# Kernel tuning notes

Measured on AMD Instinct MI355X. Metric: run time of the kernel, lower is better.

Reference implementation:

```python
import jax, jax.numpy as jnp
import numpy as np

D = 32       # hidden_size (hardcoded in AR.__init__)
H = 16       # num_heads
HD = D // H  # head_dim = 2
L = 8        # num DiT blocks
MLP = 128    # mlp_ratio 4.0
B, S, T, P = 16, 1024, 256, 32
SCALE = float(1.0 / np.sqrt(HD))


def _ln(x, g, b, eps=1e-6):
    mu = jnp.mean(x, axis=-1, keepdims=True)
    var = jnp.mean((x - mu) ** 2, axis=-1, keepdims=True)
    return (x - mu) * jax.lax.rsqrt(var + eps) * g + b


def _mha(q_in, kv_in, in_w, in_b, out_w, out_b):
    # nn.MultiheadAttention math, batch-first layout (permutation-equivalent)
    wq, wk, wv = in_w[:D], in_w[D:2 * D], in_w[2 * D:]
    bq, bk, bv = in_b[:D], in_b[D:2 * D], in_b[2 * D:]
    Bq, Sq = q_in.shape[0], q_in.shape[1]
    Sk = kv_in.shape[1]
    q = (q_in @ wq.T + bq).reshape(Bq, Sq, H, HD)
    k = (kv_in @ wk.T + bk).reshape(Bq, Sk, H, HD)
    v = (kv_in @ wv.T + bv).reshape(Bq, Sk, H, HD)
    scores = jnp.einsum('bqhd,bkhd->bhqk', q, k) * SCALE
    a = jax.nn.softmax(scores, axis=-1)
    o = jnp.einsum('bhqk,bkhd->bqhd', a, v).reshape(Bq, Sq, D)
    return o @ out_w.T + out_b


def setup_inputs() -> dict:
    key = jax.random.key(0)
    ks = iter(jax.random.split(key, 40))
    rn = lambda k, sh, sc=1.0: jax.random.normal(k, sh, jnp.float32) * sc
    inp = {
        'x': rn(next(ks), (B, S, D)),
        'speaker_emb': rn(next(ks), (B, P, D)),
        'text_phonemes': rn(next(ks), (B, T, D)),
        'timestep_emb': rn(next(ks), (B, D)),
        'mask': jnp.ones((S,), jnp.float32),
        # per-block params, stacked over L for lax.scan
        'ln1_g': jnp.ones((L, D)), 'ln1_b': jnp.zeros((L, D)),
        'ln2_g': jnp.ones((L, D)), 'ln2_b': jnp.zeros((L, D)),
        'ln22_g': jnp.ones((L, D)), 'ln22_b': jnp.zeros((L, D)),
        'ln3_g': jnp.ones((L, D)), 'ln3_b': jnp.zeros((L, D)),
        'attn_in_w': rn(next(ks), (L, 3 * D, D), 0.1), 'attn_in_b': jnp.zeros((L, 3 * D)),
        'attn_out_w': rn(next(ks), (L, D, D), 0.1), 'attn_out_b': jnp.zeros((L, D)),
        'cross_in_w': rn(next(ks), (L, 3 * D, D), 0.1), 'cross_in_b': jnp.zeros((L, 3 * D)),
        'cross_out_w': rn(next(ks), (L, D, D), 0.1), 'cross_out_b': jnp.zeros((L, D)),
        'ts_w': rn(next(ks), (L, 2 * D, D), 0.1), 'ts_b': jnp.zeros((L, 2 * D)),
        'fc1_w': rn(next(ks), (L, MLP, D), 0.1), 'fc1_b': jnp.zeros((L, MLP)),
        'fc2_w': rn(next(ks), (L, D, MLP), 0.1), 'fc2_b': jnp.zeros((L, D)),
    }
    return inp


def _forward(x, speaker_emb, text_phonemes, timestep_emb, mask, params):
    m = mask[None, :, None]  # (1, S, 1), matches mask.unsqueeze(0).unsqueeze(2)
    def body(h, p):
        h = h * m
        hn = _ln(h, p['ln1_g'], p['ln1_b'])
        h = h + _mha(hn, hn, p['attn_in_w'], p['attn_in_b'], p['attn_out_w'], p['attn_out_b'])
        # both cross attentions use cross_attn weights (cross_attn2 is dead code in source)
        ca1 = _mha(_ln(h, p['ln2_g'], p['ln2_b']), text_phonemes,
                   p['cross_in_w'], p['cross_in_b'], p['cross_out_w'], p['cross_out_b'])
        ca2 = _mha(_ln(h, p['ln22_g'], p['ln22_b']), speaker_emb,
                   p['cross_in_w'], p['cross_in_b'], p['cross_out_w'], p['cross_out_b'])
        h = h + ca1 + ca2
        ss = timestep_emb @ p['ts_w'].T + p['ts_b']        # (B, 2D)
        scale, shift = ss[:, :D], ss[:, D:]
        hm = _ln(h, p['ln3_g'], p['ln3_b']) * (1.0 + scale[:, None, :]) + shift[:, None, :]
        mlp = jax.nn.gelu(hm @ p['fc1_w'].T + p['fc1_b'], approximate=False) @ p['fc2_w'].T + p['fc2_b']
        return (h + mlp) * m, None
    out, _ = jax.lax.scan(body, x, params)
    return out


def reference(x, speaker_emb, text_phonemes, timestep_emb, mask,
              ln1_g, ln1_b, ln2_g, ln2_b, ln22_g, ln22_b, ln3_g, ln3_b,
              attn_in_w, attn_in_b, attn_out_w, attn_out_b,
              cross_in_w, cross_in_b, cross_out_w, cross_out_b,
              ts_w, ts_b, fc1_w, fc1_b, fc2_w, fc2_b):
    params = dict(ln1_g=ln1_g, ln1_b=ln1_b, ln2_g=ln2_g, ln2_b=ln2_b,
                  ln22_g=ln22_g, ln22_b=ln22_b, ln3_g=ln3_g, ln3_b=ln3_b,
                  attn_in_w=attn_in_w, attn_in_b=attn_in_b,
                  attn_out_w=attn_out_w, attn_out_b=attn_out_b,
                  cross_in_w=cross_in_w, cross_in_b=cross_in_b,
                  cross_out_w=cross_out_w, cross_out_b=cross_out_b,
                  ts_w=ts_w, ts_b=ts_b, fc1_w=fc1_w, fc1_b=fc1_b,
                  fc2_w=fc2_w, fc2_b=fc2_b)
    return _forward(x, speaker_emb, text_phonemes, timestep_emb, mask, params)
```

## Files before the change

kernel.cpp:

```cpp
#include <hip/hip_runtime.h>
#include <math.h>

#define NB 16
#define SEQ 1024
#define NT 16384
#define TT 256
#define PP 32
#define NL 8
#define SCALE 0.70710678118654752f
#define LOG2E 1.4426950408889634f
#define CS (SCALE * LOG2E)

static __device__ __forceinline__ float exp2fast(float x) {
#if __has_builtin(__builtin_amdgcn_exp2f)
  return __builtin_amdgcn_exp2f(x);
#else
  return exp2f(x);
#endif
}

__global__ __launch_bounds__(256) void k_pre(const float* __restrict__ tse,
                                             const float* __restrict__ tsw,
                                             const float* __restrict__ tsb,
                                             float* __restrict__ ssa,
                                             const float* __restrict__ text,
                                             const float* __restrict__ spk,
                                             const float* __restrict__ cw,
                                             const float* __restrict__ cb,
                                             float* __restrict__ kvtT,
                                             float* __restrict__ kvsT) {
  __shared__ float sh[64 * 33];
  int tid = threadIdx.x;
  int bx = blockIdx.x;
  if (bx < 32) {
    int idx = bx * 256 + tid;
    int l = idx >> 10;
    int rem = idx & 1023;
    int b = rem >> 6;
    int j = rem & 63;
    const float* wr = tsw + ((size_t)l * 64 + j) * 32;
    const float* xr = tse + b * 32;
    float acc = tsb[l * 64 + j];
#pragma unroll
    for (int e = 0; e < 32; e++) acc = fmaf(xr[e], wr[e], acc);
    ssa[idx] = acc;
    return;
  }
  const float* src;
  float* dst;
  int l, tok0, ntok;
  if (bx < 544) {
    l = (bx - 32) >> 6; tok0 = ((bx - 32) & 63) * 64; ntok = NB * TT; src = text;
    dst = kvtT + (size_t)l * 64 * ntok;
  } else {
    l = (bx - 544) >> 3; tok0 = ((bx - 544) & 7) * 64; ntok = NB * PP; src = spk;
    dst = kvsT + (size_t)l * 64 * ntok;
  }
  const float* w = cw + (size_t)l * 96 * 32 + 32 * 32;
  const float* wb = cb + (size_t)l * 96 + 32;
  for (int i = tid; i < 64 * 32; i += 256) {
    int tl = i >> 5, e = i & 31;
    sh[tl * 33 + e] = src[(size_t)(tok0 + tl) * 32 + e];
  }
  __syncthreads();
  int tl = tid & 63;
  int wv = tid >> 6;
#pragma unroll
  for (int k = 0; k < 16; k++) {
    int j = __builtin_amdgcn_readfirstlane(wv + 4 * k);
    const float* wr = w + j * 32;
    const float* hr = sh + tl * 33;
    float acc = wb[j];
#pragma unroll
    for (int e = 0; e < 32; e++) acc = fmaf(hr[e], wr[e], acc);
    dst[(size_t)j * ntok + tok0 + tl] = acc;
  }
}

__device__ __forceinline__ void load_row32(const float* __restrict__ base, int tok, float* r) {
#pragma unroll
  for (int e = 0; e < 32; e++) r[e] = base[(size_t)e * NT + tok];
}

__device__ __forceinline__ void ln_core(float* r) {
  float a0 = 0, a1 = 0, a2 = 0, a3 = 0;
#pragma unroll
  for (int e = 0; e < 32; e += 4) { a0 += r[e]; a1 += r[e + 1]; a2 += r[e + 2]; a3 += r[e + 3]; }
  float mu = ((a0 + a1) + (a2 + a3)) * (1.0f / 32.0f);
  float v0 = 0, v1 = 0, v2 = 0, v3 = 0;
#pragma unroll
  for (int e = 0; e < 32; e += 4) {
    float d0 = r[e] - mu, d1 = r[e + 1] - mu, d2 = r[e + 2] - mu, d3 = r[e + 3] - mu;
    v0 = fmaf(d0, d0, v0); v1 = fmaf(d1, d1, v1); v2 = fmaf(d2, d2, v2); v3 = fmaf(d3, d3, v3);
  }
  float rstd = rsqrtf(((v0 + v1) + (v2 + v3)) * (1.0f / 32.0f) + 1e-6f);
#pragma unroll
  for (int e = 0; e < 32; e++) r[e] = (r[e] - mu) * rstd;
}

__global__ __launch_bounds__(256) void k_qkv(const float* __restrict__ hin,
                                             int rowmajor,
                                             float* __restrict__ hT,
                                             const float* __restrict__ mask,
                                             const float* __restrict__ w,
                                             const float* __restrict__ wb,
                                             const float* __restrict__ g,
                                             const float* __restrict__ bv,
                                             float* __restrict__ qkvT) {
  int tid = threadIdx.x;
  int tok0 = blockIdx.x * 64;
  int yc = blockIdx.y;
  int tl = tid & 63, wv = tid >> 6;
  int tok = tok0 + tl;
  float r[32];
  if (rowmajor) {
    float m = mask[tok & (SEQ - 1)];
#pragma unroll
    for (int e = 0; e < 32; e++) r[e] = hin[(size_t)tok * 32 + e] * m;
    if (yc == 0 && wv == 0) {
#pragma unroll
      for (int e = 0; e < 32; e++) hT[(size_t)e * NT + tok] = r[e];
    }
  } else {
    load_row32(hin, tok, r);
  }
  ln_core(r);
#pragma unroll
  for (int e = 0; e < 32; e++) r[e] = fmaf(r[e], g[e], bv[e]);
#pragma unroll
  for (int k = 0; k < 6; k++) {
    int j = __builtin_amdgcn_readfirstlane(yc * 24 + wv + 4 * k);
    const float* wr = w + j * 32;
    float acc = wb[j];
#pragma unroll
    for (int e = 0; e < 32; e++) acc = fmaf(r[e], wr[e], acc);
    qkvT[(size_t)j * NT + tok] = acc;
  }
}

__global__ __launch_bounds__(256) void k_q12(const float* __restrict__ hT,
                                             const float* __restrict__ w,
                                             const float* __restrict__ wb,
                                             const float* __restrict__ g2, const float* __restrict__ b2,
                                             const float* __restrict__ g22, const float* __restrict__ b22,
                                             float* __restrict__ q1T, float* __restrict__ q2T) {
  int tid = threadIdx.x;
  int tok0 = blockIdx.x * 64, yc = blockIdx.y;
  int tl = tid & 63, wv = tid >> 6;
  int tok = tok0 + tl;
  float r[32];
  load_row32(hT, tok, r);
  ln_core(r);
  const float* g = (yc >= 2) ? g22 : g2;
  const float* bb = (yc >= 2) ? b22 : b2;
  float* dst = (yc >= 2) ? q2T : q1T;
#pragma unroll
  for (int e = 0; e < 32; e++) r[e] = fmaf(r[e], g[e], bb[e]);
  int jbase = (yc & 1) * 16;
#pragma unroll
  for (int k = 0; k < 4; k++) {
    int j = __builtin_amdgcn_readfirstlane(jbase + wv + 4 * k);
    const float* wr = w + j * 32;
    float acc = wb[j];
#pragma unroll
    for (int e = 0; e < 32; e++) acc = fmaf(r[e], wr[e], acc);
    dst[(size_t)j * NT + tok] = acc;
  }
}

__global__ __launch_bounds__(256) void k_proj_add(const float* __restrict__ s1T,
                                                  const float* __restrict__ s2T,
                                                  const float* __restrict__ w,
                                                  const float* __restrict__ wb, float bmult,
                                                  float* __restrict__ hT) {
  int tid = threadIdx.x;
  int tok0 = blockIdx.x * 64, yc = blockIdx.y;
  int tl = tid & 63, wv = tid >> 6;
  int tok = tok0 + tl;
  float r[32];
  if (s2T) {
#pragma unroll
    for (int e = 0; e < 32; e++)
      r[e] = s1T[(size_t)e * NT + tok] + s2T[(size_t)e * NT + tok];
  } else {
    load_row32(s1T, tok, r);
  }
#pragma unroll
  for (int k = 0; k < 2; k++) {
    int j = __builtin_amdgcn_readfirstlane(yc * 8 + wv + 4 * k);
    const float* wr = w + j * 32;
    float acc = bmult * wb[j];
#pragma unroll
    for (int e = 0; e < 32; e++) acc = fmaf(r[e], wr[e], acc);
    size_t gi = (size_t)j * NT + tok;
    hT[gi] += acc;
  }
}

template <int SK, int SETS>
__device__ __forceinline__ void attn_core(const float* __restrict__ qb,
                                          const float* __restrict__ kb,
                                          const float* __restrict__ vb,
                                          int kvld,
                                          float* __restrict__ ob) {
  constexpr int RPW = 4 * SETS;
  constexpr int RPB = 4 * RPW;
  constexpr int NRC = SEQ / RPB;
  int tid = threadIdx.x;
  int bx = blockIdx.x;
  int rc = bx % NRC, bh = bx / NRC;
  int b = bh >> 4, hh = bh & 15;
  int wv = tid >> 6, lane = tid & 63;
  int rg = lane >> 4, kl = lane & 15;
  int rbase = rc * RPB + wv * RPW + rg;

  const float* qxp = qb + (size_t)(2 * hh) * NT + b * SEQ;
  const float* qyp = qxp + NT;
  const float* kx = kb + (size_t)(2 * hh) * kvld + b * SK;
  const float* ky = kx + kvld;
  const float* vx = vb + (size_t)(2 * hh) * kvld + b * SK;
  const float* vy = vx + kvld;

  float qx[SETS], qy[SETS], sum[SETS], ox[SETS], oy[SETS];
#pragma unroll
  for (int s = 0; s < SETS; s++) {
    qx[s] = qxp[rbase + 4 * s] * CS;
    qy[s] = qyp[rbase + 4 * s] * CS;
    sum[s] = 0.f; ox[s] = 0.f; oy[s] = 0.f;
  }

  if constexpr (SK >= 64) {
#pragma unroll 2
    for (int c = 0; c < SK / 64; c++) {
      int o = c * 64 + kl * 4;
      float4 k4x = *(const float4*)(kx + o);
      float4 k4y = *(const float4*)(ky + o);
      float4 v4x = *(const float4*)(vx + o);
      float4 v4y = *(const float4*)(vy + o);
#pragma unroll
      for (int s = 0; s < SETS; s++) {
        float e0 = exp2fast(fmaf(qy[s], k4y.x, qx[s] * k4x.x));
        float e1 = exp2fast(fmaf(qy[s], k4y.y, qx[s] * k4x.y));
        float e2 = exp2fast(fmaf(qy[s], k4y.z, qx[s] * k4x.z));
        float e3 = exp2fast(fmaf(qy[s], k4y.w, qx[s] * k4x.w));
        sum[s] += (e0 + e1) + (e2 + e3);
        ox[s] = fmaf(e0, v4x.x, ox[s]);
        ox[s] = fmaf(e1, v4x.y, ox[s]);
        ox[s] = fmaf(e2, v4x.z, ox[s]);
        ox[s] = fmaf(e3, v4x.w, ox[s]);
        oy[s] = fmaf(e0, v4y.x, oy[s]);
        oy[s] = fmaf(e1, v4y.y, oy[s]);
        oy[s] = fmaf(e2, v4y.z, oy[s]);
        oy[s] = fmaf(e3, v4y.w, oy[s]);
      }
    }
  } else {
    float2 k2x = *(const float2*)(kx + kl * 2);
    float2 k2y = *(const float2*)(ky + kl * 2);
    float2 v2x = *(const float2*)(vx + kl * 2);
    float2 v2y = *(const float2*)(vy + kl * 2);
#pragma unroll
    for (int s = 0; s < SETS; s++) {
      float e0 = exp2fast(fmaf(qy[s], k2y.x, qx[s] * k2x.x));
      float e1 = exp2fast(fmaf(qy[s], k2y.y, qx[s] * k2x.y));
      sum[s] += e0 + e1;
      ox[s] = fmaf(e0, v2x.x, ox[s]);
      ox[s] = fmaf(e1, v2x.y, ox[s]);
      oy[s] = fmaf(e0, v2y.x, oy[s]);
      oy[s] = fmaf(e1, v2y.y, oy[s]);
    }
  }

  float* oxr = ob + (size_t)(2 * hh) * NT + b * SEQ;
  float* oyr = oxr + NT;
#pragma unroll
  for (int s = 0; s < SETS; s++) {
    float sm = sum[s];
    float o1 = ox[s];
    float o2 = oy[s];
#pragma unroll
    for (int off = 1; off < 16; off <<= 1) {
      sm += __shfl_xor(sm, off);
      o1 += __shfl_xor(o1, off);
      o2 += __shfl_xor(o2, off);
    }
    if (kl == 0) {
      float inv = 1.0f / sm;
      int r = rbase + 4 * s;
      oxr[r] = o1 * inv;
      oyr[r] = o2 * inv;
    }
  }
}

__global__ __launch_bounds__(256) void k_attn_self(const float* __restrict__ qkvT,
                                                   float* __restrict__ oT) {
  attn_core<SEQ, 8>(qkvT, qkvT + (size_t)32 * NT, qkvT + (size_t)64 * NT, NT, oT);
}

__global__ __launch_bounds__(256) void k_attn_cross(const float* __restrict__ q1T,
                                                    const float* __restrict__ q2T,
                                                    const float* __restrict__ kvt,
                                                    const float* __restrict__ kvs,
                                                    float* __restrict__ o1T,
                                                    float* __restrict__ o2T) {
  if (blockIdx.y == 0)
    attn_core<TT, 8>(q1T, kvt, kvt + (size_t)32 * (NB * TT), NB * TT, o1T);
  else
    attn_core<PP, 8>(q2T, kvs, kvs + (size_t)32 * (NB * PP), NB * PP, o2T);
}

__global__ __launch_bounds__(256) void k_fc1(const float* __restrict__ hT,
                                             const float* __restrict__ ssl,
                                             const float* __restrict__ g, const float* __restrict__ bv,
                                             const float* __restrict__ w1, const float* __restrict__ b1,
                                             float* __restrict__ uT) {
  int tid = threadIdx.x;
  int tok0 = blockIdx.x * 64, yc = blockIdx.y;
  int tl = tid & 63, wv = tid >> 6;
  int tok = tok0 + tl;
  int b = tok0 >> 10;
  const float* sc = ssl + b * 64;
  float r[32];
  load_row32(hT, tok, r);
  ln_core(r);
#pragma unroll
  for (int e = 0; e < 32; e++) {
    float ln = fmaf(r[e], g[e], bv[e]);
    r[e] = fmaf(ln, 1.0f + sc[e], sc[32 + e]);
  }
#pragma unroll
  for (int k = 0; k < 8; k++) {
    int j = __builtin_amdgcn_readfirstlane(yc * 32 + wv + 4 * k);
    const float* wr = w1 + j * 32;
    float acc = b1[j];
#pragma unroll
    for (int e = 0; e < 32; e++) acc = fmaf(r[e], wr[e], acc);
    float ge = 0.5f * acc * (1.0f + erff(acc * 0.70710678118654752f));
    uT[(size_t)j * NT + tok] = ge;
  }
}

__global__ __launch_bounds__(256) void k_fc2(const float* __restrict__ uT,
                                             float* hT,
                                             float* __restrict__ out_rm,
                                             const float* __restrict__ mask,
                                             const float* __restrict__ w2,
                                             const float* __restrict__ b2) {
  __shared__ __align__(16) float shu[64 * 132];
  int tid = threadIdx.x;
  int tok0 = blockIdx.x * 64, yc = blockIdx.y;
  for (int i = tid; i < 64 * 128; i += 256) {
    int e = i >> 6, tl = i & 63;
    shu[tl * 132 + e] = uT[(size_t)e * NT + tok0 + tl];
  }
  __syncthreads();
  int tl = tid & 63, wv = tid >> 6;
  int tok = tok0 + tl;
  int j0 = __builtin_amdgcn_readfirstlane(yc * 16 + wv);
  int j1 = __builtin_amdgcn_readfirstlane(j0 + 4);
  int j2 = __builtin_amdgcn_readfirstlane(j0 + 8);
  int j3 = __builtin_amdgcn_readfirstlane(j0 + 12);
  const float* w0 = w2 + j0 * 128;
  const float* w1 = w2 + j1 * 128;
  const float* w2r = w2 + j2 * 128;
  const float* w3 = w2 + j3 * 128;
  float a0 = b2[j0], a1 = b2[j1], a2 = b2[j2], a3 = b2[j3];
  const float4* ur = (const float4*)(shu + tl * 132);
#pragma unroll
  for (int m = 0; m < 32; m++) {
    float4 t = ur[m];
    a0 = fmaf(t.x, w0[4 * m], a0); a0 = fmaf(t.y, w0[4 * m + 1], a0);
    a0 = fmaf(t.z, w0[4 * m + 2], a0); a0 = fmaf(t.w, w0[4 * m + 3], a0);
    a1 = fmaf(t.x, w1[4 * m], a1); a1 = fmaf(t.y, w1[4 * m + 1], a1);
    a1 = fmaf(t.z, w1[4 * m + 2], a1); a1 = fmaf(t.w, w1[4 * m + 3], a1);
    a2 = fmaf(t.x, w2r[4 * m], a2); a2 = fmaf(t.y, w2r[4 * m + 1], a2);
    a2 = fmaf(t.z, w2r[4 * m + 2], a2); a2 = fmaf(t.w, w2r[4 * m + 3], a2);
    a3 = fmaf(t.x, w3[4 * m], a3); a3 = fmaf(t.y, w3[4 * m + 1], a3);
    a3 = fmaf(t.z, w3[4 * m + 2], a3); a3 = fmaf(t.w, w3[4 * m + 3], a3);
  }
  float mk = mask[tok & (SEQ - 1)];
  size_t g0 = (size_t)j0 * NT + tok, g1 = (size_t)j1 * NT + tok;
  size_t g2i = (size_t)j2 * NT + tok, g3 = (size_t)j3 * NT + tok;
  float r0 = (hT[g0] + a0) * mk;
  float r1 = (hT[g1] + a1) * mk;
  float r2 = (hT[g2i] + a2) * mk;
  float r3 = (hT[g3] + a3) * mk;
  if (out_rm) {
    out_rm[(size_t)tok * 32 + j0] = r0;
    out_rm[(size_t)tok * 32 + j1] = r1;
    out_rm[(size_t)tok * 32 + j2] = r2;
    out_rm[(size_t)tok * 32 + j3] = r3;
  } else {
    hT[g0] = r0;
    hT[g1] = r1;
    hT[g2i] = r2;
    hT[g3] = r3;
  }
}

extern "C" void kernel_launch(void* const* d_in, const int* in_sizes, int n_in,
                              void* d_out, int out_size, void* d_ws, size_t ws_size,
                              hipStream_t stream) {
  const float* x = (const float*)d_in[0];
  const float* spk = (const float*)d_in[1];
  const float* text = (const float*)d_in[2];
  const float* tse = (const float*)d_in[3];
  const float* mask = (const float*)d_in[4];
  const float* ln1_g = (const float*)d_in[5];
  const float* ln1_b = (const float*)d_in[6];
  const float* ln2_g = (const float*)d_in[7];
  const float* ln2_b = (const float*)d_in[8];
  const float* ln22_g = (const float*)d_in[9];
  const float* ln22_b = (const float*)d_in[10];
  const float* ln3_g = (const float*)d_in[11];
  const float* ln3_b = (const float*)d_in[12];
  const float* aw = (const float*)d_in[13];
  const float* ab = (const float*)d_in[14];
  const float* aow = (const float*)d_in[15];
  const float* aob = (const float*)d_in[16];
  const float* cw = (const float*)d_in[17];
  const float* cb = (const float*)d_in[18];
  const float* cow = (const float*)d_in[19];
  const float* cob = (const float*)d_in[20];
  const float* tsw = (const float*)d_in[21];
  const float* tsb = (const float*)d_in[22];
  const float* f1w = (const float*)d_in[23];
  const float* f1b = (const float*)d_in[24];
  const float* f2w = (const float*)d_in[25];
  const float* f2b = (const float*)d_in[26];

  float* ws = (float*)d_ws;
  float* hT = ws;
  float* qkvT = hT + (size_t)32 * NT;
  float* o1T = qkvT + (size_t)96 * NT;
  float* o2T = o1T + (size_t)32 * NT;
  float* q1T = o2T + (size_t)32 * NT;
  float* q2T = q1T + (size_t)32 * NT;
  float* kvtT = q2T + (size_t)32 * NT;
  float* kvsT = kvtT + (size_t)NL * 64 * (NB * TT);
  float* ssa = kvsT + (size_t)NL * 64 * (NB * PP);
  float* uT = o1T;

  k_pre<<<608, 256, 0, stream>>>(tse, tsw, tsb, ssa, text, spk, cw, cb, kvtT, kvsT);

  for (int l = 0; l < NL; l++) {
    k_qkv<<<dim3(256, 4), 256, 0, stream>>>((l == 0) ? x : hT, (l == 0) ? 1 : 0, hT, mask,
                                            aw + (size_t)l * 96 * 32, ab + l * 96,
                                            ln1_g + l * 32, ln1_b + l * 32, qkvT);
    k_attn_self<<<2048, 256, 0, stream>>>(qkvT, o1T);
    k_proj_add<<<dim3(256, 4), 256, 0, stream>>>(o1T, nullptr,
                                                 aow + (size_t)l * 32 * 32, aob + l * 32, 1.0f, hT);
    k_q12<<<dim3(256, 4), 256, 0, stream>>>(hT, cw + (size_t)l * 96 * 32, cb + l * 96,
                                            ln2_g + l * 32, ln2_b + l * 32,
                                            ln22_g + l * 32, ln22_b + l * 32, q1T, q2T);
    k_attn_cross<<<dim3(2048, 2), 256, 0, stream>>>(q1T, q2T,
                                                    kvtT + (size_t)l * 64 * (NB * TT),
                                                    kvsT + (size_t)l * 64 * (NB * PP),
                                                    o1T, o2T);
    k_proj_add<<<dim3(256, 4), 256, 0, stream>>>(o1T, o2T,
                                                 cow + (size_t)l * 32 * 32, cob + l * 32, 2.0f, hT);
    k_fc1<<<dim3(256, 4), 256, 0, stream>>>(hT, ssa + (size_t)l * NB * 64,
                                            ln3_g + l * 32, ln3_b + l * 32,
                                            f1w + (size_t)l * 128 * 32, f1b + l * 128, uT);
    k_fc2<<<dim3(256, 2), 256, 0, stream>>>(uT, hT, (l == NL - 1) ? (float*)d_out : nullptr,
                                            mask, f2w + (size_t)l * 32 * 128, f2b + l * 32);
  }
}
```

Baseline: 971.3 us.

## Fuse attention output projections into following LN+Q and LN+FC1 kernels

Merges the self-attention out-projection with the cross-attention Q projections, and the cross-attention out-projection with the LN3/modulation/FC1/GELU stage. Each fused block stages 32 tokens of the residual and attention output in shared memory, so two kernel launches per layer and their residual-stream round trips are removed. The residual buffers are ping-ponged (hS → hB → hS) and the workspace layout is reshuffled to allow this. In exchange, the projection work is recomputed in every y-slice of the grid. The self-attention key loop also gets hoisted float4 base pointers and unroll 4.

```diff
diff --git a/kernel.cpp b/kernel.cpp
--- a/kernel.cpp
+++ b/kernel.cpp
@@ -138,62 +138,115 @@
   }
 }
 
-__global__ __launch_bounds__(256) void k_q12(const float* __restrict__ hT,
-                                             const float* __restrict__ w,
-                                             const float* __restrict__ wb,
-                                             const float* __restrict__ g2, const float* __restrict__ b2,
-                                             const float* __restrict__ g22, const float* __restrict__ b22,
-                                             float* __restrict__ q1T, float* __restrict__ q2T) {
-  int tid = threadIdx.x;
-  int tok0 = blockIdx.x * 64, yc = blockIdx.y;
-  int tl = tid & 63, wv = tid >> 6;
-  int tok = tok0 + tl;
+__global__ __launch_bounds__(256) void k_projq12(const float* __restrict__ hA,
+                                                 const float* __restrict__ oT,
+                                                 const float* __restrict__ aow,
+                                                 const float* __restrict__ aob,
+                                                 float* __restrict__ hB,
+                                                 const float* __restrict__ cwq,
+                                                 const float* __restrict__ cbq,
+                                                 const float* __restrict__ g2, const float* __restrict__ b2,
+                                                 const float* __restrict__ g22, const float* __restrict__ b22,
+                                                 float* __restrict__ q1T,
+                                                 float* __restrict__ q2T) {
+  __shared__ float sh[32 * 33];
+  __shared__ float so[32 * 33];
+  int tid = threadIdx.x;
+  int tok0 = blockIdx.x * 32;
+  int y = blockIdx.y;
+  for (int i = tid; i < 1024; i += 256) {
+    int e = i >> 5, t = i & 31;
+    sh[t * 33 + e] = hA[(size_t)e * NT + tok0 + t];
+    so[t * 33 + e] = oT[(size_t)e * NT + tok0 + t];
+  }
+  __syncthreads();
+  int tl = tid & 31, jg = tid >> 5;
+#pragma unroll
+  for (int kk = 0; kk < 4; kk++) {
+    int j = jg + 8 * kk;
+    const float* wr = aow + j * 32;
+    float acc = aob[j];
+#pragma unroll
+    for (int i = 0; i < 32; i++) acc = fmaf(so[tl * 33 + i], wr[i], acc);
+    float hp = sh[tl * 33 + j] + acc;
+    sh[tl * 33 + j] = hp;
+    if (y == 0) hB[(size_t)j * NT + tok0 + tl] = hp;
+  }
+  __syncthreads();
   float r[32];
-  load_row32(hT, tok, r);
+#pragma unroll
+  for (int i = 0; i < 32; i++) r[i] = sh[tl * 33 + i];
   ln_core(r);
-  const float* g = (yc >= 2) ? g22 : g2;
-  const float* bb = (yc >= 2) ? b22 : b2;
-  float* dst = (yc >= 2) ? q2T : q1T;
-#pragma unroll
-  for (int e = 0; e < 32; e++) r[e] = fmaf(r[e], g[e], bb[e]);
-  int jbase = (yc & 1) * 16;
-#pragma unroll
-  for (int k = 0; k < 4; k++) {
-    int j = __builtin_amdgcn_readfirstlane(jbase + wv + 4 * k);
-    const float* wr = w + j * 32;
-    float acc = wb[j];
-#pragma unroll
-    for (int e = 0; e < 32; e++) acc = fmaf(r[e], wr[e], acc);
-    dst[(size_t)j * NT + tok] = acc;
-  }
-}
-
-__global__ __launch_bounds__(256) void k_proj_add(const float* __restrict__ s1T,
-                                                  const float* __restrict__ s2T,
-                                                  const float* __restrict__ w,
-                                                  const float* __restrict__ wb, float bmult,
-                                                  float* __restrict__ hT) {
-  int tid = threadIdx.x;
-  int tok0 = blockIdx.x * 64, yc = blockIdx.y;
-  int tl = tid & 63, wv = tid >> 6;
-  int tok = tok0 + tl;
+  const float* g = y ? g22 : g2;
+  const float* bb = y ? b22 : b2;
+  float* dst = y ? q2T : q1T;
+#pragma unroll
+  for (int i = 0; i < 32; i++) r[i] = fmaf(r[i], g[i], bb[i]);
+#pragma unroll
+  for (int kk = 0; kk < 4; kk++) {
+    int j = jg + 8 * kk;
+    const float* wr = cwq + j * 32;
+    float acc = cbq[j];
+#pragma unroll
+    for (int i = 0; i < 32; i++) acc = fmaf(r[i], wr[i], acc);
+    dst[(size_t)j * NT + tok0 + tl] = acc;
+  }
+}
+
+__global__ __launch_bounds__(256) void k_projfc1(const float* __restrict__ hBp,
+                                                 const float* __restrict__ o1T,
+                                                 const float* __restrict__ o2T,
+                                                 const float* __restrict__ cow,
+                                                 const float* __restrict__ cob,
+                                                 float* __restrict__ hC,
+                                                 const float* __restrict__ ssl,
+                                                 const float* __restrict__ g3, const float* __restrict__ b3,
+                                                 const float* __restrict__ w1, const float* __restrict__ b1,
+                                                 float* __restrict__ uT) {
+  __shared__ float sh[32 * 33];
+  __shared__ float so[32 * 33];
+  int tid = threadIdx.x;
+  int tok0 = blockIdx.x * 32;
+  int yc = blockIdx.y;
+  for (int i = tid; i < 1024; i += 256) {
+    int e = i >> 5, t = i & 31;
+    sh[t * 33 + e] = hBp[(size_t)e * NT + tok0 + t];
+    so[t * 33 + e] = o1T[(size_t)e * NT + tok0 + t] + o2T[(size_t)e * NT + tok0 + t];
+  }
+  __syncthreads();
+  int tl = tid & 31, jg = tid >> 5;
+#pragma unroll
+  for (int kk = 0; kk < 4; kk++) {
+    int j = jg + 8 * kk;
+    const float* wr = cow + j * 32;
+    float acc = 2.0f * cob[j];
+#pragma unroll
+    for (int i = 0; i < 32; i++) acc = fmaf(so[tl * 33 + i], wr[i], acc);
+    float hp = sh[tl * 33 + j] + acc;
+    sh[tl * 33 + j] = hp;
+    if (yc == 0) hC[(size_t)j * NT + tok0 + tl] = hp;
+  }
+  __syncthreads();
   float r[32];
-  if (s2T) {
-#pragma unroll
-    for (int e = 0; e < 32; e++)
-      r[e] = s1T[(size_t)e * NT + tok] + s2T[(size_t)e * NT + tok];
-  } else {
-    load_row32(s1T, tok, r);
-  }
-#pragma unroll
-  for (int k = 0; k < 2; k++) {
-    int j = __builtin_amdgcn_readfirstlane(yc * 8 + wv + 4 * k);
-    const float* wr = w + j * 32;
-    float acc = bmult * wb[j];
-#pragma unroll
-    for (int e = 0; e < 32; e++) acc = fmaf(r[e], wr[e], acc);
-    size_t gi = (size_t)j * NT + tok;
-    hT[gi] += acc;
+#pragma unroll
+  for (int i = 0; i < 32; i++) r[i] = sh[tl * 33 + i];
+  ln_core(r);
+  int b = tok0 >> 10;
+  const float* sc = ssl + b * 64;
+#pragma unroll
+  for (int i = 0; i < 32; i++) {
+    float ln = fmaf(r[i], g3[i], b3[i]);
+    r[i] = fmaf(ln, 1.0f + sc[i], sc[32 + i]);
+  }
+#pragma unroll
+  for (int kk = 0; kk < 4; kk++) {
+    int j = yc * 32 + jg + 8 * kk;
+    const float* wr = w1 + j * 32;
+    float acc = b1[j];
+#pragma unroll
+    for (int i = 0; i < 32; i++) acc = fmaf(r[i], wr[i], acc);
+    float ge = 0.5f * acc * (1.0f + erff(acc * 0.70710678118654752f));
+    uT[(size_t)j * NT + tok0 + tl] = ge;
   }
 }
 
@@ -230,13 +283,16 @@
   }
 
   if constexpr (SK >= 64) {
-#pragma unroll 2
+    const float4* kx4 = (const float4*)(kx + kl * 4);
+    const float4* ky4 = (const float4*)(ky + kl * 4);
+    const float4* vx4 = (const float4*)(vx + kl * 4);
+    const float4* vy4 = (const float4*)(vy + kl * 4);
+#pragma unroll 4
     for (int c = 0; c < SK / 64; c++) {
-      int o = c * 64 + kl * 4;
-      float4 k4x = *(const float4*)(kx + o);
-      float4 k4y = *(const float4*)(ky + o);
-      float4 v4x = *(const float4*)(vx + o);
-      float4 v4y = *(const float4*)(vy + o);
+      float4 k4x = kx4[c * 16];
+      float4 k4y = ky4[c * 16];
+      float4 v4x = vx4[c * 16];
+      float4 v4y = vy4[c * 16];
 #pragma unroll
       for (int s = 0; s < SETS; s++) {
         float e0 = exp2fast(fmaf(qy[s], k4y.x, qx[s] * k4x.x));
@@ -308,37 +364,6 @@
     attn_core<TT, 8>(q1T, kvt, kvt + (size_t)32 * (NB * TT), NB * TT, o1T);
   else
     attn_core<PP, 8>(q2T, kvs, kvs + (size_t)32 * (NB * PP), NB * PP, o2T);
-}
-
-__global__ __launch_bounds__(256) void k_fc1(const float* __restrict__ hT,
-                                             const float* __restrict__ ssl,
-                                             const float* __restrict__ g, const float* __restrict__ bv,
-                                             const float* __restrict__ w1, const float* __restrict__ b1,
-                                             float* __restrict__ uT) {
-  int tid = threadIdx.x;
-  int tok0 = blockIdx.x * 64, yc = blockIdx.y;
-  int tl = tid & 63, wv = tid >> 6;
-  int tok = tok0 + tl;
-  int b = tok0 >> 10;
-  const float* sc = ssl + b * 64;
-  float r[32];
-  load_row32(hT, tok, r);
-  ln_core(r);
-#pragma unroll
-  for (int e = 0; e < 32; e++) {
-    float ln = fmaf(r[e], g[e], bv[e]);
-    r[e] = fmaf(ln, 1.0f + sc[e], sc[32 + e]);
-  }
-#pragma unroll
-  for (int k = 0; k < 8; k++) {
-    int j = __builtin_amdgcn_readfirstlane(yc * 32 + wv + 4 * k);
-    const float* wr = w1 + j * 32;
-    float acc = b1[j];
-#pragma unroll
-    for (int e = 0; e < 32; e++) acc = fmaf(r[e], wr[e], acc);
-    float ge = 0.5f * acc * (1.0f + erff(acc * 0.70710678118654752f));
-    uT[(size_t)j * NT + tok] = ge;
-  }
 }
 
 __global__ __launch_bounds__(256) void k_fc2(const float* __restrict__ uT,
@@ -431,39 +456,42 @@
   const float* f2b = (const float*)d_in[26];
 
   float* ws = (float*)d_ws;
-  float* hT = ws;
-  float* qkvT = hT + (size_t)32 * NT;
-  float* o1T = qkvT + (size_t)96 * NT;
-  float* o2T = o1T + (size_t)32 * NT;
-  float* q1T = o2T + (size_t)32 * NT;
-  float* q2T = q1T + (size_t)32 * NT;
-  float* kvtT = q2T + (size_t)32 * NT;
+  const size_t SL = (size_t)32 * NT;
+  float* hS = ws;
+  float* qkvT = ws + SL;
+  float* q1T = ws + 2 * SL;
+  float* q2T = ws + 3 * SL;
+  float* oS = ws + 4 * SL;
+  float* hB = ws + SL;
+  float* o1c = ws + 6 * SL;
+  float* o2c = ws + 7 * SL;
+  float* uT = ws + 2 * SL;
+  float* kvtT = ws + 8 * SL;
   float* kvsT = kvtT + (size_t)NL * 64 * (NB * TT);
   float* ssa = kvsT + (size_t)NL * 64 * (NB * PP);
-  float* uT = o1T;
 
   k_pre<<<608, 256, 0, stream>>>(tse, tsw, tsb, ssa, text, spk, cw, cb, kvtT, kvsT);
 
   for (int l = 0; l < NL; l++) {
-    k_qkv<<<dim3(256, 4), 256, 0, stream>>>((l == 0) ? x : hT, (l == 0) ? 1 : 0, hT, mask,
+    k_qkv<<<dim3(256, 4), 256, 0, stream>>>((l == 0) ? x : hS, (l == 0) ? 1 : 0, hS, mask,
                                             aw + (size_t)l * 96 * 32, ab + l * 96,
                                             ln1_g + l * 32, ln1_b + l * 32, qkvT);
-    k_attn_self<<<2048, 256, 0, stream>>>(qkvT, o1T);
-    k_proj_add<<<dim3(256, 4), 256, 0, stream>>>(o1T, nullptr,
-                                                 aow + (size_t)l * 32 * 32, aob + l * 32, 1.0f, hT);
-    k_q12<<<dim3(256, 4), 256, 0, stream>>>(hT, cw + (size_t)l * 96 * 32, cb + l * 96,
-                                            ln2_g + l * 32, ln2_b + l * 32,
-                                            ln22_g + l * 32, ln22_b + l * 32, q1T, q2T);
+    k_attn_self<<<2048, 256, 0, stream>>>(qkvT, oS);
+    k_projq12<<<dim3(512, 2), 256, 0, stream>>>(hS, oS,
+                                                aow + (size_t)l * 32 * 32, aob + l * 32, hB,
+                                                cw + (size_t)l * 96 * 32, cb + l * 96,
+                                                ln2_g + l * 32, ln2_b + l * 32,
+                                                ln22_g + l * 32, ln22_b + l * 32, q1T, q2T);
     k_attn_cross<<<dim3(2048, 2), 256, 0, stream>>>(q1T, q2T,
                                                     kvtT + (size_t)l * 64 * (NB * TT),
                                                     kvsT + (size_t)l * 64 * (NB * PP),
-                                                    o1T, o2T);
-    k_proj_add<<<dim3(256, 4), 256, 0, stream>>>(o1T, o2T,
-                                                 cow + (size_t)l * 32 * 32, cob + l * 32, 2.0f, hT);
-    k_fc1<<<dim3(256, 4), 256, 0, stream>>>(hT, ssa + (size_t)l * NB * 64,
-                                            ln3_g + l * 32, ln3_b + l * 32,
-                                            f1w + (size_t)l * 128 * 32, f1b + l * 128, uT);
-    k_fc2<<<dim3(256, 2), 256, 0, stream>>>(uT, hT, (l == NL - 1) ? (float*)d_out : nullptr,
+                                                    o1c, o2c);
+    k_projfc1<<<dim3(512, 4), 256, 0, stream>>>(hB, o1c, o2c,
+                                                cow + (size_t)l * 32 * 32, cob + l * 32, hS,
+                                                ssa + (size_t)l * NB * 64,
+                                                ln3_g + l * 32, ln3_b + l * 32,
+                                                f1w + (size_t)l * 128 * 32, f1b + l * 128, uT);
+    k_fc2<<<dim3(256, 2), 256, 0, stream>>>(uT, hS, (l == NL - 1) ? (float*)d_out : nullptr,
                                             mask, f2w + (size_t)l * 32 * 128, f2b + l * 32);
   }
 }
```

New measurement: 1.063 ms. 9.4% more time.
